# Performance work log

Hardware: AMD Instinct MI355X
Metric: run time of the kernel (lower is better)

The kernel has to match this reference:

```python
import jax, jax.numpy as jnp
import numpy as np

B, S, IN_DIM, OUT_DIM = 4, 2048, 1024, 1024
NEG = -9e15

def _xavier(key, shape, gain=1.414):
    fan_in, fan_out = shape[0], shape[1]
    a = gain * np.sqrt(6.0 / (fan_in + fan_out))
    return jax.random.uniform(key, shape, jnp.float32, -a, a)

def setup_inputs() -> dict:
    key = jax.random.key(0)
    ks = jax.random.split(key, 8)
    x = jax.random.normal(ks[0], (B, S, IN_DIM), jnp.float32)
    W_query = _xavier(ks[1], (IN_DIM, OUT_DIM))
    W_key = _xavier(ks[2], (IN_DIM, OUT_DIM))
    W_value = _xavier(ks[3], (IN_DIM, OUT_DIM))
    # torch Linear default init (kaiming-uniform-ish); values don't matter for correctness baseline
    W1 = _xavier(ks[4], (OUT_DIM + IN_DIM, OUT_DIM), gain=1.0)
    b1 = jnp.zeros((OUT_DIM,), jnp.float32)
    W2 = _xavier(ks[5], (OUT_DIM, OUT_DIM), gain=1.0)
    b2 = jnp.zeros((OUT_DIM,), jnp.float32)
    return {"x": x, "W_query": W_query, "W_key": W_key, "W_value": W_value,
            "W1": W1, "b1": b1, "W2": W2, "b2": b2}

def reference(x, W_query, W_key, W_value, W1, b1, W2, b2):
    # QKV projections: [B,S,in] @ [in,out] -> [B,S,out]
    q = jnp.einsum('bsi,io->bso', x, W_query)
    k = jnp.einsum('bsi,io->bso', x, W_key)
    v = jnp.einsum('bsi,io->bso', x, W_value)
    scale = 1.0 / jnp.sqrt(jnp.float32(OUT_DIM))
    e = jnp.einsum('bqd,bkd->bqk', q, k) * scale  # [B,S,S]
    causal = jnp.tril(jnp.ones((S, S), jnp.float32))  # mask > 0 keeps lower triangle
    attn = jnp.where(causal > 0, e, jnp.float32(NEG))
    attn = jax.nn.softmax(attn, axis=2)
    # dropout: eval mode (train=False) -> identity
    out = jnp.einsum('bqk,bkd->bqd', attn, v)  # [B,S,out]
    h = jnp.concatenate([out, x], axis=-1)  # [B,S,out+in]
    h = jax.nn.relu(jnp.einsum('bsf,fo->bso', h, W1) + b1)
    return jnp.einsum('bsf,fo->bso', h, W2) + b2
```

## Files before the change

### kernel.cpp

```cpp
#include <hip/hip_runtime.h>
#include <stdint.h>

typedef __attribute__((ext_vector_type(8))) short short8;
typedef __attribute__((ext_vector_type(4))) short short4v;
typedef __attribute__((ext_vector_type(4))) float f32x4;

__device__ __forceinline__ unsigned short f32_to_bf16(float f) {
    unsigned int u = __float_as_uint(f);
    u += 0x7FFFu + ((u >> 16) & 1u);
    return (unsigned short)(u >> 16);
}

__device__ __forceinline__ short8 load8_f32_as_bf16(const float* __restrict__ ap) {
    f32x4 f0 = *(const f32x4*)ap;
    f32x4 f1 = *(const f32x4*)(ap + 4);
    union { short8 s; unsigned short u[8]; } cv;
#pragma unroll
    for (int t = 0; t < 4; ++t) {
        cv.u[t]     = f32_to_bf16(f0[t]);
        cv.u[t + 4] = f32_to_bf16(f1[t]);
    }
    return cv.s;
}

__device__ __forceinline__ void gld_lds16(const void* g, void* l) {
    __builtin_amdgcn_global_load_lds(
        (const __attribute__((address_space(1))) unsigned int*)(unsigned long long)(uintptr_t)g,
        (__attribute__((address_space(3))) unsigned int*)(unsigned int)(uintptr_t)l,
        16, 0, 0);
}

template<int AMODE, int EPI, int SWIZ, bool KLIMIT, int MT>
__global__ __launch_bounds__(256, 4)
void gemm128(const unsigned short* __restrict__ A, const unsigned short* __restrict__ A2,
             int lda, int lda2, int ksplit,
             const unsigned short* __restrict__ B, int ldb,
             void* __restrict__ C, int ldc, int K,
             long aStride, long bStride, long cStride,
             const float* __restrict__ bias, long biasStride, float scale,
             void* __restrict__ C2, int ldc2)
{
    int z = blockIdx.z;
    int mblk, nblk;
    if (SWIZ == 1) {
        int lin = blockIdx.y * gridDim.x + blockIdx.x;
        int mchunk = gridDim.y >> 3;
        int xcd = lin & 7, idx = lin >> 3;
        mblk = xcd * mchunk + idx % mchunk;
        nblk = idx / mchunk;
    } else if (SWIZ == 5) {
        int x = blockIdx.x;
        int per = (int)gridDim.x >> 3;
        x = (x & 7) * per + (x >> 3);
        int a = (int)sqrtf(2.f * (float)x + 1.f);
        if (a > 15) a = 15;
        while (a < 15 && ((a + 1) * (a + 2) / 2) <= x) ++a;
        while (a > 0 && (a * (a + 1) / 2) > x) --a;
        mblk = a;
        nblk = x - a * (a + 1) / 2;
    } else if (SWIZ == 6) {
        int x = blockIdx.x, yy = blockIdx.y;
        if (z < 2) { mblk = x * 8 + (yy & 7); nblk = yy >> 3; }
        else       { nblk = x * 8 + (yy & 7); mblk = yy >> 3; }
    } else if (SWIZ == 7) {
        int glin = (int)blockIdx.z * 128 + (int)blockIdx.y * 8 + (int)blockIdx.x;
        int xcd = glin & 7;
        int s   = glin >> 3;
        z = xcd >> 1;
        int h  = xcd & 1;
        int jm = s & 7;
        nblk   = s >> 3;
        mblk   = (jm & 1) ? (15 - h - (jm >> 1) * 2) : ((jm >> 1) * 2 + h);
    } else {
        mblk = blockIdx.y;
        nblk = blockIdx.x;
    }
    int m0 = mblk * MT;
    int n0 = nblk * 128;

    const unsigned short* Ab;
    const unsigned short* Bb;
    if (SWIZ == 6) {
        if (z < 2) { Ab = A; Bb = B + (size_t)z * bStride; }
        else       { Ab = B + (size_t)2 * bStride; Bb = A; }
    } else {
        Ab = A + (size_t)z * aStride;
        Bb = B + (size_t)z * bStride;
    }

    __shared__ __align__(16) short As[MT * 64];
    __shared__ __align__(16) short Bs[128 * 64];

    int tid  = threadIdx.x;
    int lane = tid & 63, wid = tid >> 6;
    constexpr int MI = MT / 32;
    int wm = (wid & 1) * (MT / 2), wn = (wid >> 1) * 64;
    int fr = lane & 15, fq = lane >> 4;
    int sw0 = ((fq    ) ^ (fr & 7)) * 16;
    int sw1 = ((fq ^ 4) ^ (fr & 7)) * 16;

    int rS = tid >> 3;
    int cS = ((tid & 7) ^ (rS & 7)) * 8;
    char* AsB = (char*)As; char* BsB = (char*)Bs;

    int kend = KLIMIT ? min(K, m0 + MT) : K;

    f32x4 acc[MI][4];
#pragma unroll
    for (int i = 0; i < MI; ++i)
#pragma unroll
    for (int j = 0; j < 4; ++j) acc[i][j] = f32x4{0.f, 0.f, 0.f, 0.f};

    for (int k0 = 0; k0 < kend; k0 += 64) {
        const unsigned short* Asrc = Ab;
        int koff = k0, ldax = lda;
        if (AMODE == 2 && k0 >= ksplit) { Asrc = A2; koff = k0 - ksplit; ldax = lda2; }
        const unsigned short* pa = Asrc + (size_t)(m0 + rS) * ldax + koff + cS;
        const unsigned short* pb = Bb   + (size_t)(n0 + rS) * ldb  + k0   + cS;
#pragma unroll
        for (int t = 0; t < MT / 32; ++t)
            gld_lds16(pa + (size_t)(32 * t) * ldax, AsB + t * 4096 + tid * 16);
#pragma unroll
        for (int t = 0; t < 4; ++t)
            gld_lds16(pb + (size_t)(32 * t) * ldb,  BsB + t * 4096 + tid * 16);
        __syncthreads();

#pragma unroll
        for (int kh = 0; kh < 2; ++kh) {
            int sw = kh ? sw1 : sw0;
            short8 a[MI], b[4];
#pragma unroll
            for (int i = 0; i < MI; ++i)
                a[i] = *(const short8*)(AsB + (wm + i * 16 + fr) * 128 + sw);
#pragma unroll
            for (int j = 0; j < 4; ++j)
                b[j] = *(const short8*)(BsB + (wn + j * 16 + fr) * 128 + sw);
#pragma unroll
            for (int i = 0; i < MI; ++i)
#pragma unroll
            for (int j = 0; j < 4; ++j)
                acc[i][j] = __builtin_amdgcn_mfma_f32_16x16x32_bf16(a[i], b[j], acc[i][j], 0, 0, 0);
        }
        __syncthreads();
    }

    if (EPI == 0) {
        unsigned short* Cz; int ldcz;
        if (SWIZ == 6 && z >= 2) { Cz = (unsigned short*)C2; ldcz = ldc2; }
        else { Cz = (unsigned short*)C + (size_t)z * cStride; ldcz = ldc; }
#pragma unroll
        for (int i = 0; i < MI; ++i)
#pragma unroll
        for (int j = 0; j < 4; ++j)
#pragma unroll
        for (int r = 0; r < 4; ++r) {
            int row = m0 + wm + i * 16 + fq * 4 + r;
            int col = n0 + wn + j * 16 + fr;
            Cz[(size_t)row * ldcz + col] = f32_to_bf16(acc[i][j][r]);
        }
    } else if (EPI == 6) {
        unsigned short* Cz = (unsigned short*)C + (size_t)z * cStride;
        float* rs = const_cast<float*>(bias) + z * biasStride;
#pragma unroll
        for (int i = 0; i < MI; ++i)
#pragma unroll
        for (int r = 0; r < 4; ++r) {
            int row = m0 + wm + i * 16 + fq * 4 + r;
            float s = 0.f;
#pragma unroll
            for (int j = 0; j < 4; ++j) {
                int col = n0 + wn + j * 16 + fr;
                float e = (col <= row) ? __expf(acc[i][j][r] * scale - 16.f) : 0.f;
                s += e;
                Cz[(size_t)row * ldc + col] = f32_to_bf16(e);
            }
            s += __shfl_xor(s, 1);
            s += __shfl_xor(s, 2);
            s += __shfl_xor(s, 4);
            s += __shfl_xor(s, 8);
            if (fr == 0) atomicAdd(&rs[row], s);
        }
    } else if (EPI == 4) {
        unsigned short* Cz = (unsigned short*)C + (size_t)z * cStride;
#pragma unroll
        for (int i = 0; i < MI; ++i)
#pragma unroll
        for (int r = 0; r < 4; ++r) {
            int row = m0 + wm + i * 16 + fq * 4 + r;
            float inv = 1.f / bias[z * biasStride + row];
#pragma unroll
            for (int j = 0; j < 4; ++j) {
                int col = n0 + wn + j * 16 + fr;
                Cz[(size_t)row * ldc + col] = f32_to_bf16(acc[i][j][r] * inv);
            }
        }
    } else {
#pragma unroll
        for (int i = 0; i < MI; ++i)
#pragma unroll
        for (int j = 0; j < 4; ++j)
#pragma unroll
        for (int r = 0; r < 4; ++r) {
            int row = m0 + wm + i * 16 + fq * 4 + r;
            int col = n0 + wn + j * 16 + fr;
            float v = acc[i][j][r];
            if (EPI == 2) {
                v += bias[col];
                v = v > 0.f ? v : 0.f;
                ((unsigned short*)C + (size_t)z * cStride)[(size_t)row * ldc + col] = f32_to_bf16(v);
            } else {
                ((float*)C + (size_t)z * cStride)[(size_t)row * ldc + col] = v + bias[col];
            }
        }
    }
}

__device__ __forceinline__ void transpose_tile64(const float* __restrict__ in,
                                                 unsigned short* __restrict__ out,
                                                 int rows, int cols, int bx, int by, int tid)
{
    __shared__ float t[64][65];
    int tx = tid & 15, ty = tid >> 4;
    int r0 = by * 64, c0 = bx * 64;
#pragma unroll
    for (int i = 0; i < 4; ++i) {
        f32x4 v = *(const f32x4*)(in + (size_t)(r0 + ty + i * 16) * cols + c0 + tx * 4);
#pragma unroll
        for (int j = 0; j < 4; ++j) t[ty + i * 16][tx * 4 + j] = v[j];
    }
    __syncthreads();
#pragma unroll
    for (int i = 0; i < 4; ++i) {
        union { short4v s; unsigned short u[4]; } o;
#pragma unroll
        for (int j = 0; j < 4; ++j) o.u[j] = f32_to_bf16(t[tx * 4 + j][ty + i * 16]);
        *(short4v*)(out + (size_t)(c0 + ty + i * 16) * rows + r0 + tx * 4) = o.s;
    }
}

__global__ __launch_bounds__(256)
void prep_kernel(const float* __restrict__ x,
                 const float* __restrict__ Wq, const float* __restrict__ Wk,
                 const float* __restrict__ Wv, const float* __restrict__ W1,
                 const float* __restrict__ W2,
                 unsigned short* __restrict__ xb, unsigned short* __restrict__ WT,
                 unsigned short* __restrict__ W1T, unsigned short* __restrict__ W2T,
                 float* __restrict__ rsum)
{
    int idx = blockIdx.x;
    int tid = threadIdx.x;
    if (idx < 1024) {
#pragma unroll
        for (int it = 0; it < 4; ++it) {
            size_t i = ((size_t)idx * 4 + it) * 2048 + (size_t)tid * 8;
            *(short8*)(xb + i) = load8_f32_as_bf16(x + i);
        }
    } else if (idx < 1792) {
        int t = idx - 1024;
        int w = t >> 8; t &= 255;
        const float* in = w == 0 ? Wq : (w == 1 ? Wk : Wv);
        transpose_tile64(in, WT + (size_t)w * 1024 * 1024, 1024, 1024,
                         t & 15, t >> 4, tid);
    } else if (idx < 2304) {
        int t = idx - 1792;
        transpose_tile64(W1, W1T, 2048, 1024, t & 15, t >> 4, tid);
    } else if (idx < 2560) {
        int t = idx - 2304;
        transpose_tile64(W2, W2T, 1024, 1024, t & 15, t >> 4, tid);
    } else {
        int t = idx - 2560;
        f32x4 zero = {0.f, 0.f, 0.f, 0.f};
        float* p = rsum + ((size_t)t * 256 + tid) * 8;
        *(f32x4*)p = zero;
        *(f32x4*)(p + 4) = zero;
    }
}

extern "C" void kernel_launch(void* const* d_in, const int* in_sizes, int n_in,
                              void* d_out, int out_size, void* d_ws, size_t ws_size,
                              hipStream_t stream)
{
    const float* x  = (const float*)d_in[0];
    const float* Wq = (const float*)d_in[1];
    const float* Wk = (const float*)d_in[2];
    const float* Wv = (const float*)d_in[3];
    const float* W1 = (const float*)d_in[4];
    const float* b1 = (const float*)d_in[5];
    const float* W2 = (const float*)d_in[6];
    const float* b2 = (const float*)d_in[7];
    float* out = (float*)d_out;

    size_t off = 0;
    auto alloc = [&](size_t bytes) {
        char* r = (char*)d_ws + off;
        off += (bytes + 255) & ~(size_t)255;
        return r;
    };
    const size_t TOK = (size_t)8192 * 1024;
    unsigned short* WT   = (unsigned short*)alloc((size_t)3072 * 1024 * 2);
    unsigned short* W1T  = (unsigned short*)alloc((size_t)1024 * 2048 * 2);
    unsigned short* W2T  = (unsigned short*)alloc((size_t)1024 * 1024 * 2);
    unsigned short* xb   = (unsigned short*)alloc(TOK * 2);
    unsigned short* vT   = (unsigned short*)alloc((size_t)1024 * 8192 * 2);
    unsigned short* attn = (unsigned short*)alloc(TOK * 2);
    float*          rsum = (float*)         alloc((size_t)4 * 2048 * 4);
    unsigned short* q    = (unsigned short*)alloc(TOK * 2);
    unsigned short* k    = (unsigned short*)alloc(TOK * 2);
    unsigned short* S    = (unsigned short*)alloc((size_t)4 * 2048 * 2048 * 2);
    unsigned short* h1   = S;

    prep_kernel<<<2564, 256, 0, stream>>>(x, Wq, Wk, Wv, W1, W2, xb, WT, W1T, W2T, rsum);

    gemm128<0, 0, 6, false, 128><<<dim3(8, 64, 3), 256, 0, stream>>>(
        xb, nullptr, 1024, 0, 0, WT, 1024, q, 1024, 1024,
        0, (long)1024 * 1024, (long)TOK, nullptr, 0, 0.f, vT, 8192);

    gemm128<0, 6, 5, false, 128><<<dim3(136, 1, 4), 256, 0, stream>>>(
        q, nullptr, 1024, 0, 0, k, 1024, S, 2048, 1024,
        (long)2048 * 1024, (long)2048 * 1024, (long)2048 * 2048, rsum, 2048, 0.03125f,
        nullptr, 0);
    gemm128<0, 4, 7, true, 128><<<dim3(8, 16, 4), 256, 0, stream>>>(
        S, nullptr, 2048, 0, 0, vT, 8192, attn, 1024, 2048,
        (long)2048 * 2048, (long)2048, (long)2048 * 1024, rsum, 2048, 0.f, nullptr, 0);

    gemm128<2, 2, 1, false, 128><<<dim3(8, 64, 1), 256, 0, stream>>>(
        attn, xb, 1024, 1024, 1024, W1T, 2048, h1, 1024, 2048, 0, 0, 0, b1, 0, 0.f,
        nullptr, 0);
    gemm128<0, 3, 1, false, 128><<<dim3(8, 64, 1), 256, 0, stream>>>(
        h1, nullptr, 1024, 0, 0, W2T, 1024, out, 1024, 1024, 0, 0, 0, b2, 0, 0.f,
        nullptr, 0);
}
```

Baseline: 289.9 us.

## Add double-buffered LDS GEMM kernel for attention and MLP stages

```diff
diff --git a/kernel.cpp b/kernel.cpp
--- a/kernel.cpp
+++ b/kernel.cpp
@@ -39,6 +39,111 @@
              long aStride, long bStride, long cStride,
              const float* __restrict__ bias, long biasStride, float scale,
              void* __restrict__ C2, int ldc2)
+{
+    int z = blockIdx.z;
+    int mblk, nblk;
+    if (SWIZ == 6) {
+        int x = blockIdx.x, yy = blockIdx.y;
+        if (z < 2) { mblk = x * 8 + (yy & 7); nblk = yy >> 3; }
+        else       { nblk = x * 8 + (yy & 7); mblk = yy >> 3; }
+    } else {
+        mblk = blockIdx.y;
+        nblk = blockIdx.x;
+    }
+    int m0 = mblk * MT;
+    int n0 = nblk * 128;
+
+    const unsigned short* Ab;
+    const unsigned short* Bb;
+    if (SWIZ == 6) {
+        if (z < 2) { Ab = A; Bb = B + (size_t)z * bStride; }
+        else       { Ab = B + (size_t)2 * bStride; Bb = A; }
+    } else {
+        Ab = A + (size_t)z * aStride;
+        Bb = B + (size_t)z * bStride;
+    }
+
+    __shared__ __align__(16) short As[MT * 64];
+    __shared__ __align__(16) short Bs[128 * 64];
+
+    int tid  = threadIdx.x;
+    int lane = tid & 63, wid = tid >> 6;
+    constexpr int MI = MT / 32;
+    int wm = (wid & 1) * (MT / 2), wn = (wid >> 1) * 64;
+    int fr = lane & 15, fq = lane >> 4;
+    int sw0 = ((fq    ) ^ (fr & 7)) * 16;
+    int sw1 = ((fq ^ 4) ^ (fr & 7)) * 16;
+
+    int rS = tid >> 3;
+    int cS = ((tid & 7) ^ (rS & 7)) * 8;
+    char* AsB = (char*)As; char* BsB = (char*)Bs;
+
+    int kend = KLIMIT ? min(K, m0 + MT) : K;
+
+    f32x4 acc[MI][4];
+#pragma unroll
+    for (int i = 0; i < MI; ++i)
+#pragma unroll
+    for (int j = 0; j < 4; ++j) acc[i][j] = f32x4{0.f, 0.f, 0.f, 0.f};
+
+    for (int k0 = 0; k0 < kend; k0 += 64) {
+        const unsigned short* Asrc = Ab;
+        int koff = k0, ldax = lda;
+        if (AMODE == 2 && k0 >= ksplit) { Asrc = A2; koff = k0 - ksplit; ldax = lda2; }
+        const unsigned short* pa = Asrc + (size_t)(m0 + rS) * ldax + koff + cS;
+        const unsigned short* pb = Bb   + (size_t)(n0 + rS) * ldb  + k0   + cS;
+#pragma unroll
+        for (int t = 0; t < MT / 32; ++t)
+            gld_lds16(pa + (size_t)(32 * t) * ldax, AsB + t * 4096 + tid * 16);
+#pragma unroll
+        for (int t = 0; t < 4; ++t)
+            gld_lds16(pb + (size_t)(32 * t) * ldb,  BsB + t * 4096 + tid * 16);
+        __syncthreads();
+
+#pragma unroll
+        for (int kh = 0; kh < 2; ++kh) {
+            int sw = kh ? sw1 : sw0;
+            short8 a[MI], b[4];
+#pragma unroll
+            for (int i = 0; i < MI; ++i)
+                a[i] = *(const short8*)(AsB + (wm + i * 16 + fr) * 128 + sw);
+#pragma unroll
+            for (int j = 0; j < 4; ++j)
+                b[j] = *(const short8*)(BsB + (wn + j * 16 + fr) * 128 + sw);
+#pragma unroll
+            for (int i = 0; i < MI; ++i)
+#pragma unroll
+            for (int j = 0; j < 4; ++j)
+                acc[i][j] = __builtin_amdgcn_mfma_f32_16x16x32_bf16(a[i], b[j], acc[i][j], 0, 0, 0);
+        }
+        __syncthreads();
+    }
+
+    if (EPI == 0) {
+        unsigned short* Cz; int ldcz;
+        if (SWIZ == 6 && z >= 2) { Cz = (unsigned short*)C2; ldcz = ldc2; }
+        else { Cz = (unsigned short*)C + (size_t)z * cStride; ldcz = ldc; }
+#pragma unroll
+        for (int i = 0; i < MI; ++i)
+#pragma unroll
+        for (int j = 0; j < 4; ++j)
+#pragma unroll
+        for (int r = 0; r < 4; ++r) {
+            int row = m0 + wm + i * 16 + fq * 4 + r;
+            int col = n0 + wn + j * 16 + fr;
+            Cz[(size_t)row * ldcz + col] = f32_to_bf16(acc[i][j][r]);
+        }
+    }
+}
+
+template<int AMODE, int EPI, int SWIZ, bool KLIMIT>
+__global__ __launch_bounds__(256, 2)
+void gemmdb(const unsigned short* __restrict__ A, const unsigned short* __restrict__ A2,
+            int lda, int lda2, int ksplit,
+            const unsigned short* __restrict__ B, int ldb,
+            void* __restrict__ C, int ldc, int K,
+            long aStride, long bStride, long cStride,
+            const float* __restrict__ bias, long biasStride, float scale)
 {
     int z = blockIdx.z;
     int mblk, nblk;
@@ -58,10 +163,6 @@
         while (a > 0 && (a * (a + 1) / 2) > x) --a;
         mblk = a;
         nblk = x - a * (a + 1) / 2;
-    } else if (SWIZ == 6) {
-        int x = blockIdx.x, yy = blockIdx.y;
-        if (z < 2) { mblk = x * 8 + (yy & 7); nblk = yy >> 3; }
-        else       { nblk = x * 8 + (yy & 7); mblk = yy >> 3; }
     } else if (SWIZ == 7) {
         int glin = (int)blockIdx.z * 128 + (int)blockIdx.y * 8 + (int)blockIdx.x;
         int xcd = glin & 7;
@@ -75,94 +176,87 @@
         mblk = blockIdx.y;
         nblk = blockIdx.x;
     }
-    int m0 = mblk * MT;
+    int m0 = mblk * 128;
     int n0 = nblk * 128;
 
-    const unsigned short* Ab;
-    const unsigned short* Bb;
-    if (SWIZ == 6) {
-        if (z < 2) { Ab = A; Bb = B + (size_t)z * bStride; }
-        else       { Ab = B + (size_t)2 * bStride; Bb = A; }
-    } else {
-        Ab = A + (size_t)z * aStride;
-        Bb = B + (size_t)z * bStride;
-    }
-
-    __shared__ __align__(16) short As[MT * 64];
-    __shared__ __align__(16) short Bs[128 * 64];
+    const unsigned short* Ab = A + (size_t)z * aStride;
+    const unsigned short* Bb = B + (size_t)z * bStride;
+
+    __shared__ __align__(16) char lds[65536];
 
     int tid  = threadIdx.x;
     int lane = tid & 63, wid = tid >> 6;
-    constexpr int MI = MT / 32;
-    int wm = (wid & 1) * (MT / 2), wn = (wid >> 1) * 64;
+    int wm = (wid & 1) * 64, wn = (wid >> 1) * 64;
     int fr = lane & 15, fq = lane >> 4;
     int sw0 = ((fq    ) ^ (fr & 7)) * 16;
     int sw1 = ((fq ^ 4) ^ (fr & 7)) * 16;
 
     int rS = tid >> 3;
     int cS = ((tid & 7) ^ (rS & 7)) * 8;
-    char* AsB = (char*)As; char* BsB = (char*)Bs;
-
-    int kend = KLIMIT ? min(K, m0 + MT) : K;
-
-    f32x4 acc[MI][4];
-#pragma unroll
-    for (int i = 0; i < MI; ++i)
+
+    int kend = KLIMIT ? min(K, m0 + 128) : K;
+    int NT = kend >> 6;
+
+    f32x4 acc[4][4];
+#pragma unroll
+    for (int i = 0; i < 4; ++i)
 #pragma unroll
     for (int j = 0; j < 4; ++j) acc[i][j] = f32x4{0.f, 0.f, 0.f, 0.f};
 
-    for (int k0 = 0; k0 < kend; k0 += 64) {
-        const unsigned short* Asrc = Ab;
-        int koff = k0, ldax = lda;
-        if (AMODE == 2 && k0 >= ksplit) { Asrc = A2; koff = k0 - ksplit; ldax = lda2; }
+    auto STAGE = [&](int kt) {
+        char* dst = lds + (kt & 1) * 32768;
+        const unsigned short* Asrc = Ab; int koff = kt << 6; int ldax = lda;
+        if (AMODE == 2 && koff >= ksplit) { Asrc = A2; koff -= ksplit; ldax = lda2; }
         const unsigned short* pa = Asrc + (size_t)(m0 + rS) * ldax + koff + cS;
-        const unsigned short* pb = Bb   + (size_t)(n0 + rS) * ldb  + k0   + cS;
-#pragma unroll
-        for (int t = 0; t < MT / 32; ++t)
-            gld_lds16(pa + (size_t)(32 * t) * ldax, AsB + t * 4096 + tid * 16);
-#pragma unroll
-        for (int t = 0; t < 4; ++t)
-            gld_lds16(pb + (size_t)(32 * t) * ldb,  BsB + t * 4096 + tid * 16);
-        __syncthreads();
-
+        const unsigned short* pb = Bb   + (size_t)(n0 + rS) * ldb + (kt << 6) + cS;
+#pragma unroll
+        for (int u = 0; u < 4; ++u)
+            gld_lds16(pa + (size_t)(32 * u) * ldax, dst + u * 4096 + tid * 16);
+#pragma unroll
+        for (int u = 0; u < 4; ++u)
+            gld_lds16(pb + (size_t)(32 * u) * ldb, dst + 16384 + u * 4096 + tid * 16);
+    };
+
+    STAGE(0);
+    for (int t = 0; t < NT; ++t) {
+        if (t + 1 < NT) {
+            STAGE(t + 1);
+            asm volatile("s_waitcnt vmcnt(8)" ::: "memory");
+        } else {
+            asm volatile("s_waitcnt vmcnt(0)" ::: "memory");
+        }
+        __builtin_amdgcn_s_barrier();
+        __builtin_amdgcn_sched_barrier(0);
+        const char* AsB = (const char*)lds + (t & 1) * 32768;
+        const char* BsB = AsB + 16384;
 #pragma unroll
         for (int kh = 0; kh < 2; ++kh) {
             int sw = kh ? sw1 : sw0;
-            short8 a[MI], b[4];
-#pragma unroll
-            for (int i = 0; i < MI; ++i)
+            short8 a[4], b[4];
+#pragma unroll
+            for (int i = 0; i < 4; ++i)
                 a[i] = *(const short8*)(AsB + (wm + i * 16 + fr) * 128 + sw);
 #pragma unroll
             for (int j = 0; j < 4; ++j)
                 b[j] = *(const short8*)(BsB + (wn + j * 16 + fr) * 128 + sw);
-#pragma unroll
-            for (int i = 0; i < MI; ++i)
+            __builtin_amdgcn_s_setprio(1);
+#pragma unroll
+            for (int i = 0; i < 4; ++i)
 #pragma unroll
             for (int j = 0; j < 4; ++j)
                 acc[i][j] = __builtin_amdgcn_mfma_f32_16x16x32_bf16(a[i], b[j], acc[i][j], 0, 0, 0);
-        }
-        __syncthreads();
-    }
-
-    if (EPI == 0) {
-        unsigned short* Cz; int ldcz;
-        if (SWIZ == 6 && z >= 2) { Cz = (unsigned short*)C2; ldcz = ldc2; }
-        else { Cz = (unsigned short*)C + (size_t)z * cStride; ldcz = ldc; }
-#pragma unroll
-        for (int i = 0; i < MI; ++i)
-#pragma unroll
-        for (int j = 0; j < 4; ++j)
-#pragma unroll
-        for (int r = 0; r < 4; ++r) {
-            int row = m0 + wm + i * 16 + fq * 4 + r;
-            int col = n0 + wn + j * 16 + fr;
-            Cz[(size_t)row * ldcz + col] = f32_to_bf16(acc[i][j][r]);
-        }
-    } else if (EPI == 6) {
+            __builtin_amdgcn_s_setprio(0);
+        }
+        __builtin_amdgcn_s_barrier();
+        __builtin_amdgcn_sched_barrier(0);
+        asm volatile("" ::: "memory");
+    }
+
+    if (EPI == 6) {
         unsigned short* Cz = (unsigned short*)C + (size_t)z * cStride;
         float* rs = const_cast<float*>(bias) + z * biasStride;
 #pragma unroll
-        for (int i = 0; i < MI; ++i)
+        for (int i = 0; i < 4; ++i)
 #pragma unroll
         for (int r = 0; r < 4; ++r) {
             int row = m0 + wm + i * 16 + fq * 4 + r;
@@ -183,7 +277,7 @@
     } else if (EPI == 4) {
         unsigned short* Cz = (unsigned short*)C + (size_t)z * cStride;
 #pragma unroll
-        for (int i = 0; i < MI; ++i)
+        for (int i = 0; i < 4; ++i)
 #pragma unroll
         for (int r = 0; r < 4; ++r) {
             int row = m0 + wm + i * 16 + fq * 4 + r;
@@ -196,7 +290,7 @@
         }
     } else {
 #pragma unroll
-        for (int i = 0; i < MI; ++i)
+        for (int i = 0; i < 4; ++i)
 #pragma unroll
         for (int j = 0; j < 4; ++j)
 #pragma unroll
@@ -315,18 +409,19 @@
         xb, nullptr, 1024, 0, 0, WT, 1024, q, 1024, 1024,
         0, (long)1024 * 1024, (long)TOK, nullptr, 0, 0.f, vT, 8192);
 
-    gemm128<0, 6, 5, false, 128><<<dim3(136, 1, 4), 256, 0, stream>>>(
+    gemmdb<0, 6, 5, false><<<dim3(136, 1, 4), 256, 0, stream>>>(
         q, nullptr, 1024, 0, 0, k, 1024, S, 2048, 1024,
-        (long)2048 * 1024, (long)2048 * 1024, (long)2048 * 2048, rsum, 2048, 0.03125f,
-        nullptr, 0);
-    gemm128<0, 4, 7, true, 128><<<dim3(8, 16, 4), 256, 0, stream>>>(
+        (long)2048 * 1024, (long)2048 * 1024, (long)2048 * 2048, rsum, 2048, 0.03125f);
+
+    gemmdb<0, 4, 7, true><<<dim3(8, 16, 4), 256, 0, stream>>>(
         S, nullptr, 2048, 0, 0, vT, 8192, attn, 1024, 2048,
-        (long)2048 * 2048, (long)2048, (long)2048 * 1024, rsum, 2048, 0.f, nullptr, 0);
-
-    gemm128<2, 2, 1, false, 128><<<dim3(8, 64, 1), 256, 0, stream>>>(
-        attn, xb, 1024, 1024, 1024, W1T, 2048, h1, 1024, 2048, 0, 0, 0, b1, 0, 0.f,
-        nullptr, 0);
-    gemm128<0, 3, 1, false, 128><<<dim3(8, 64, 1), 256, 0, stream>>>(
-        h1, nullptr, 1024, 0, 0, W2T, 1024, out, 1024, 1024, 0, 0, 0, b2, 0, 0.f,
-        nullptr, 0);
-}
+        (long)2048 * 2048, (long)2048, (long)2048 * 1024, rsum, 2048, 0.f);
+
+    gemmdb<2, 2, 1, false><<<dim3(8, 64, 1), 256, 0, stream>>>(
+        attn, xb, 1024, 1024, 1024, W1T, 2048, h1, 1024, 2048,
+        0, 0, 0, b1, 0, 0.f);
+
+    gemmdb<0, 3, 1, false><<<dim3(8, 64, 1), 256, 0, stream>>>(
+        h1, nullptr, 1024, 0, 0, W2T, 1024, out, 1024, 1024,
+        0, 0, 0, b2, 0, 0.f);
+}
```

Result: no change. 287.5 us (-0.8%).
